# Kernel optimization log

Hardware: AMD Instinct MI355X
Metric: run time of the kernel (lower is better)

## Reference

```python
import jax, jax.numpy as jnp
import numpy as np

HID = 2048; H = 16; QLR = 1536; KVLR = 512
DN = 128; DR = 64; DV = 128; DQ = DN + DR  # 192
B = 2; S = 2048
THETA = 10000.0; EPS = 1e-6


def rms_norm(x, w, eps=EPS):
    x32 = x.astype(jnp.float32)
    var = jnp.mean(x32 * x32, axis=-1, keepdims=True)
    return (w * (x32 * jax.lax.rsqrt(var + eps))).astype(x.dtype)


def rotate_half(x):
    x1, x2 = jnp.split(x, 2, axis=-1)
    return jnp.concatenate((-x2, x1), axis=-1)


def rope_tables(seq_len, dim, base=THETA):
    inv_freq = 1.0 / (base ** (jnp.arange(0, dim, 2, dtype=jnp.float32) / dim))
    t = jnp.arange(seq_len, dtype=jnp.float32)
    freqs = jnp.outer(t, inv_freq)            # [S, dim/2]
    emb = jnp.concatenate((freqs, freqs), -1)  # [S, dim]
    return jnp.cos(emb), jnp.sin(emb)


def setup_inputs() -> dict:
    key = jax.random.key(0)
    ks = jax.random.split(key, 8)
    sd = lambda fan_in: 1.0 / np.sqrt(fan_in)
    return {
        "hidden_states": jax.random.normal(ks[0], (B, S, HID), jnp.float32),
        "w_qa": jax.random.normal(ks[1], (QLR, HID), jnp.float32) * sd(HID),
        "q_a_ln_w": jnp.ones((QLR,), jnp.float32),
        "w_qb": jax.random.normal(ks[2], (H * DQ, QLR), jnp.float32) * sd(QLR),
        "w_kva": jax.random.normal(ks[3], (KVLR + DR, HID), jnp.float32) * sd(HID),
        "kv_a_ln_w": jnp.ones((KVLR,), jnp.float32),
        "w_kvb": jax.random.normal(ks[4], (H * (DN + DV), KVLR), jnp.float32) * sd(KVLR),
        "w_o": jax.random.normal(ks[5], (HID, H * DV), jnp.float32) * sd(H * DV),
    }


def reference(hidden_states, w_qa, q_a_ln_w, w_qb, w_kva, kv_a_ln_w, w_kvb, w_o):
    b, s, _ = hidden_states.shape
    scale = DQ ** -0.5
    cos, sin = rope_tables(s, DR)  # [S, DR] each

    # Q path: low-rank down-proj -> RMSNorm -> up-proj
    cq = rms_norm(hidden_states @ w_qa.T, q_a_ln_w)            # [B,S,QLR]
    q = (cq @ w_qb.T).reshape(b, s, H, DQ).transpose(0, 2, 1, 3)  # [B,H,S,DQ]
    q_nope, q_pe = q[..., :DN], q[..., DN:]
    q_pe = q_pe * cos + rotate_half(q_pe) * sin

    # KV path: joint compressed kv + shared rope key
    ckv = hidden_states @ w_kva.T                               # [B,S,KVLR+DR]
    k_pe = ckv[..., KVLR:].reshape(b, s, 1, DR).transpose(0, 2, 1, 3)  # [B,1,S,DR]
    k_pe = k_pe * cos + rotate_half(k_pe) * sin
    ckv_l = rms_norm(ckv[..., :KVLR], kv_a_ln_w)                # [B,S,KVLR]
    kv = (ckv_l @ w_kvb.T).reshape(b, s, H, DN + DV).transpose(0, 2, 1, 3)
    k_nope, v = kv[..., :DN], kv[..., DN:]                      # [B,H,S,DN],[B,H,S,DV]

    q_full = jnp.concatenate([q_nope, q_pe], axis=-1)           # [B,H,S,DQ]
    k_full = jnp.concatenate(
        [k_nope, jnp.broadcast_to(k_pe, (b, H, s, DR))], axis=-1)

    scores = jnp.einsum('bhqd,bhkd->bhqk', q_full, k_full) * scale
    causal = jnp.triu(jnp.ones((s, s), dtype=bool), k=1)
    scores = jnp.where(causal, -jnp.inf, scores)
    attn = jax.nn.softmax(scores.astype(jnp.float32), axis=-1).astype(q_full.dtype)

    out = jnp.einsum('bhqk,bhkd->bhqd', attn, v)                # [B,H,S,DV]
    out = out.transpose(0, 2, 1, 3).reshape(b, s, H * DV)
    return out @ w_o.T
```

## Files before the change

kernel.cpp:

```cpp
#include <hip/hip_runtime.h>
#include <stdint.h>
#include <stddef.h>

typedef unsigned short u16;
typedef short s16x8 __attribute__((ext_vector_type(8)));
typedef unsigned short u16x4 __attribute__((ext_vector_type(4)));
typedef unsigned short u16x8 __attribute__((ext_vector_type(8)));
typedef float f32x4 __attribute__((ext_vector_type(4)));

__device__ __forceinline__ u16 f2b(float f) {
  uint32_t u = __builtin_bit_cast(uint32_t, f);
  uint32_t r = u + 0x7fffu + ((u >> 16) & 1u);
  return (u16)(r >> 16);
}
__device__ __forceinline__ float b2f(u16 h) {
  uint32_t u = ((uint32_t)h) << 16;
  return __builtin_bit_cast(float, u);
}
__device__ __forceinline__ void gl_lds16(const void* g, void* l) {
  __builtin_amdgcn_global_load_lds((const __attribute__((address_space(1))) void*)g,
                                   (__attribute__((address_space(3))) void*)l,
                                   16, 0, 0);
}

__global__ __launch_bounds__(256) void cast_k(const float* __restrict__ in,
                                              u16* __restrict__ out, int n4) {
  int i = blockIdx.x * 256 + threadIdx.x;
  if (i >= n4) return;
  float4 v = ((const float4*)in)[i];
  u16x4 o; o[0]=f2b(v.x); o[1]=f2b(v.y); o[2]=f2b(v.z); o[3]=f2b(v.w);
  ((u16x4*)out)[i] = o;
}

__global__ __launch_bounds__(256) void cast_pad_k(const float* __restrict__ in,
                                                  u16* __restrict__ out,
                                                  int Kd, int nvalid, int n4) {
  int i = blockIdx.x * 256 + threadIdx.x;
  if (i >= n4) return;
  int row = (i << 2) / Kd;
  u16x4 o;
  if (row < nvalid) {
    float4 v = ((const float4*)in)[i];
    o[0]=f2b(v.x); o[1]=f2b(v.y); o[2]=f2b(v.z); o[3]=f2b(v.w);
  } else {
    o[0]=0; o[1]=0; o[2]=0; o[3]=0;
  }
  ((u16x4*)out)[i] = o;
}

template<int MODE>
__global__ __launch_bounds__(256) void gemm_bt(const u16* __restrict__ A,
                                               const u16* __restrict__ B,
                                               void* __restrict__ Cv,
                                               int M, int N, int K) {
  __shared__ u16 As[128 * 32];
  __shared__ u16 Bs[128 * 32];
  const int t = threadIdx.x;
  const int w = t >> 6, l = t & 63;
  const int nb = N >> 7;
  const int cpx = gridDim.x >> 3;
  const int swz = (blockIdx.x & 7) * cpx + (blockIdx.x >> 3);
  const int bm = (swz / nb) << 7;
  const int bn = (swz % nb) << 7;
  const int wr = (w >> 1) << 6;
  const int wc = (w & 1) << 6;
  const int Kh = K / gridDim.y;
  const int ks0 = blockIdx.y * Kh;

  f32x4 acc[4][4];
  #pragma unroll
  for (int i = 0; i < 4; i++)
    #pragma unroll
    for (int j = 0; j < 4; j++) acc[i][j] = (f32x4){0.f, 0.f, 0.f, 0.f};

  const u16* ga = A + (size_t)(bm + w * 32 + (l >> 2)) * K + ks0 + ((l & 3) * 8);
  const u16* gb = B + (size_t)(bn + w * 32 + (l >> 2)) * K + ks0 + ((l & 3) * 8);
  u16* la0 = &As[(w * 32) * 32];
  u16* la1 = &As[(w * 32 + 16) * 32];
  u16* lb0 = &Bs[(w * 32) * 32];
  u16* lb1 = &Bs[(w * 32 + 16) * 32];

  for (int k0 = 0; k0 < Kh; k0 += 32) {
    __syncthreads();
    gl_lds16(ga, la0);
    gl_lds16(ga + (size_t)16 * K, la1);
    gl_lds16(gb, lb0);
    gl_lds16(gb + (size_t)16 * K, lb1);
    ga += 32; gb += 32;
    __syncthreads();

    s16x8 af[4], bf[4];
    #pragma unroll
    for (int i = 0; i < 4; i++) {
      af[i] = *(const s16x8*)&As[(wr + i * 16 + (l & 15)) * 32 + (l >> 4) * 8];
      bf[i] = *(const s16x8*)&Bs[(wc + i * 16 + (l & 15)) * 32 + (l >> 4) * 8];
    }
    #pragma unroll
    for (int mi = 0; mi < 4; mi++)
      #pragma unroll
      for (int ni = 0; ni < 4; ni++)
        acc[mi][ni] = __builtin_amdgcn_mfma_f32_16x16x32_bf16(af[mi], bf[ni], acc[mi][ni], 0, 0, 0);
  }

  #pragma unroll
  for (int mi = 0; mi < 4; mi++)
    #pragma unroll
    for (int ni = 0; ni < 4; ni++) {
      int row0 = bm + wr + mi * 16 + ((l >> 4) << 2);
      int col  = bn + wc + ni * 16 + (l & 15);
      #pragma unroll
      for (int r = 0; r < 4; r++) {
        float v = acc[mi][ni][r];
        size_t idx = (size_t)(row0 + r) * N + col;
        if (MODE == 1)      ((u16*)Cv)[idx] = f2b(v);
        else if (MODE == 0) ((float*)Cv)[idx] = v;
        else                atomicAdd((float*)Cv + idx, v);
      }
    }
}

__global__ __launch_bounds__(256) void rmsnorm_k(const float* __restrict__ X,
                                                 const float* __restrict__ W,
                                                 u16* __restrict__ Y, int ldx, int D) {
  const int row = blockIdx.x;
  const float* x = X + (size_t)row * ldx;
  const int t = threadIdx.x;
  float ss = 0.f;
  for (int i = t; i < (D >> 2); i += 256) {
    float4 v = ((const float4*)x)[i];
    ss += v.x * v.x + v.y * v.y + v.z * v.z + v.w * v.w;
  }
  #pragma unroll
  for (int off = 32; off > 0; off >>= 1) ss += __shfl_xor(ss, off);
  __shared__ float red[4];
  if ((t & 63) == 0) red[t >> 6] = ss;
  __syncthreads();
  float tot = red[0] + red[1] + red[2] + red[3];
  float r = rsqrtf(tot / (float)D + 1e-6f);
  u16* y = Y + (size_t)row * D;
  for (int i = t; i < (D >> 2); i += 256) {
    float4 v = ((const float4*)x)[i];
    float4 g = ((const float4*)W)[i];
    u16x4 o;
    o[0] = f2b(v.x * r * g.x); o[1] = f2b(v.y * r * g.y);
    o[2] = f2b(v.z * r * g.z); o[3] = f2b(v.w * r * g.w);
    ((u16x4*)y)[i] = o;
  }
}

__global__ __launch_bounds__(256) void rope_kpe_k(const float* __restrict__ CQ,
                                                  u16* __restrict__ Kpe) {
  int idx = blockIdx.x * 256 + threadIdx.x;
  if (idx >= 4096 * 32) return;
  int d = idx & 31;
  int m = idx >> 5;
  int s = m & 2047;
  float inv = expf(-(float)(2 * d) * (9.210340371976184f / 64.0f));
  float ang = (float)s * inv;
  float sn, c;
  sincosf(ang, &sn, &c);
  float x1 = CQ[(size_t)m * 2176 + 2048 + d];
  float x2 = CQ[(size_t)m * 2176 + 2080 + d];
  Kpe[m * 64 + d]      = f2b(x1 * c - x2 * sn);
  Kpe[m * 64 + 32 + d] = f2b(x2 * c + x1 * sn);
}

__global__ __launch_bounds__(256) void rope_q_k(u16* __restrict__ Qb) {
  int idx = blockIdx.x * 256 + threadIdx.x;
  if (idx >= 4096 * 16 * 32) return;
  int d = idx & 31;
  int h = (idx >> 5) & 15;
  int m = idx >> 9;
  int s = m & 2047;
  float inv = expf(-(float)(2 * d) * (9.210340371976184f / 64.0f));
  float ang = (float)s * inv;
  float sn, c;
  sincosf(ang, &sn, &c);
  size_t base = (size_t)m * 3072 + h * 192 + 128 + d;
  float x1 = b2f(Qb[base]);
  float x2 = b2f(Qb[base + 32]);
  Qb[base]      = f2b(x1 * c - x2 * sn);
  Qb[base + 32] = f2b(x2 * c + x1 * sn);
}

__global__ __launch_bounds__(256) void vt_k(const u16* __restrict__ KV,
                                            u16* __restrict__ VT) {
  __shared__ u16 L[64][72];
  const int t = threadIdx.x;
  const int s_t = blockIdx.x & 31;
  const int d_t = (blockIdx.x >> 5) & 1;
  const int bh  = blockIdx.x >> 6;
  const int h = bh & 15, b = bh >> 4;
  const size_t bS = (size_t)b * 2048;
  const int s0 = s_t << 6, d0 = d_t << 6;

  #pragma unroll
  for (int i = 0; i < 2; i++) {
    int rs = (t >> 3) + i * 32;
    int ch = t & 7;
    u16x8 v = *(const u16x8*)&KV[(bS + s0 + rs) * 4096 + h * 256 + 128 + d0 + ch * 8];
    *(u16x8*)&L[rs][ch * 8] = v;
  }
  __syncthreads();
  #pragma unroll
  for (int i = 0; i < 2; i++) {
    int rd = (t >> 3) + i * 32;
    int ch = t & 7;
    u16x8 o;
    #pragma unroll
    for (int j = 0; j < 8; j++) o[j] = L[ch * 8 + j][rd];
    *(u16x8*)&VT[((size_t)bh * 128 + d0 + rd) * 2048 + s0 + ch * 8] = o;
  }
}

__global__ __launch_bounds__(256) void attn4_k(const u16* __restrict__ Q,
                                               const u16* __restrict__ KV,
                                               const u16* __restrict__ Kpe,
                                               const u16* __restrict__ VT,
                                               u16* __restrict__ O) {
  const float SCALE = 0.07216878364870322f;
  const int t = threadIdx.x, w = t >> 6, l = t & 63;
  const int bh = blockIdx.x & 31;
  const int qt = 31 - (blockIdx.x >> 5);
  const int h = bh & 15, b = bh >> 4;
  const int q0 = qt << 6;
  const size_t bS = (size_t)b * 2048;

  __shared__ u16 Kl[2][64 * 192];
  __shared__ u16 Pl[4][16][72];

  s16x8 qf[6];
  {
    const u16* qp = Q + (bS + q0 + w * 16 + (l & 15)) * 3072 + h * 192 + ((l >> 4) * 8);
    #pragma unroll
    for (int c = 0; c < 6; c++) qf[c] = *(const s16x8*)(qp + c * 32);
  }
  float m_i[4] = {-1e30f, -1e30f, -1e30f, -1e30f};
  float lp[4]  = {0.f, 0.f, 0.f, 0.f};
  f32x4 accO[8];
  #pragma unroll
  for (int i = 0; i < 8; i++) accO[i] = (f32x4){0.f, 0.f, 0.f, 0.f};

  const u16* vbp = VT + (size_t)bh * 128 * 2048;
  const int ktiles = qt + 1;

  auto STAGE = [&](int buf, int k0) {
    #pragma unroll
    for (int it = 0; it < 6; ++it) {
      int sl = it * 64 + l;
      int r = w * 16 + sl / 24;
      int cc = (sl % 24) ^ (r & 7);
      const u16* src = (cc < 16)
          ? KV + (bS + k0 + r) * 4096 + h * 256 + cc * 8
          : Kpe + (bS + k0 + r) * 64 + (cc - 16) * 8;
      gl_lds16(src, &Kl[buf][w * 3072 + it * 512]);
    }
  };

  STAGE(0, 0);
  __syncthreads();

  int cur = 0;
  for (int kt = 0; kt < ktiles; ++kt) {
    const int k0 = kt << 6;

    s16x8 va[8], vb[8];
    #pragma unroll
    for (int df = 0; df < 8; df++)
      va[df] = *(const s16x8*)&vbp[(size_t)(df * 16 + (l & 15)) * 2048 + k0 + (l >> 4) * 8];
    #pragma unroll
    for (int df = 0; df < 8; df++)
      vb[df] = *(const s16x8*)&vbp[(size_t)(df * 16 + (l & 15)) * 2048 + k0 + 32 + (l >> 4) * 8];

    if (kt + 1 < ktiles) STAGE(cur ^ 1, k0 + 64);

    f32x4 sa[4];
    #pragma unroll
    for (int cf = 0; cf < 4; cf++) sa[cf] = (f32x4){0.f, 0.f, 0.f, 0.f};
    __builtin_amdgcn_s_setprio(1);
    #pragma unroll
    for (int c = 0; c < 6; c++) {
      #pragma unroll
      for (int cf = 0; cf < 4; cf++) {
        int row = cf * 16 + (l & 15);
        int ch = (c * 4 + (l >> 4)) ^ (row & 7);
        s16x8 kf = *(const s16x8*)&Kl[cur][row * 192 + ch * 8];
        sa[cf] = __builtin_amdgcn_mfma_f32_16x16x32_bf16(qf[c], kf, sa[cf], 0, 0, 0);
      }
    }
    __builtin_amdgcn_s_setprio(0);

    const bool diag = (kt == qt);
    #pragma unroll
    for (int cf = 0; cf < 4; cf++)
      #pragma unroll
      for (int r = 0; r < 4; r++) {
        float s = sa[cf][r] * SCALE;
        if (diag) {
          int qrow = q0 + w * 16 + ((l >> 4) << 2) + r;
          if (k0 + cf * 16 + (l & 15) > qrow) s = -1e30f;
        }
        sa[cf][r] = s;
      }

    float lm[4];
    #pragma unroll
    for (int r = 0; r < 4; r++)
      lm[r] = fmaxf(fmaxf(sa[0][r], sa[1][r]), fmaxf(sa[2][r], sa[3][r]));
    bool safe = (lm[0] <= m_i[0] + 8.f) && (lm[1] <= m_i[1] + 8.f) &&
                (lm[2] <= m_i[2] + 8.f) && (lm[3] <= m_i[3] + 8.f);
    if (!__all(safe)) {
      #pragma unroll
      for (int r = 0; r < 4; r++) {
        float mx = lm[r];
        #pragma unroll
        for (int dd = 1; dd < 16; dd <<= 1) mx = fmaxf(mx, __shfl_xor(mx, dd));
        float mnew = fmaxf(m_i[r], mx);
        float alpha = __expf(m_i[r] - mnew);
        m_i[r] = mnew;
        lp[r] *= alpha;
        #pragma unroll
        for (int df = 0; df < 8; df++) accO[df][r] *= alpha;
      }
    }
    #pragma unroll
    for (int r = 0; r < 4; r++) {
      float e0 = __expf(sa[0][r] - m_i[r]);
      float e1 = __expf(sa[1][r] - m_i[r]);
      float e2 = __expf(sa[2][r] - m_i[r]);
      float e3 = __expf(sa[3][r] - m_i[r]);
      lp[r] += (e0 + e1) + (e2 + e3);
      int prow = ((l >> 4) << 2) + r;
      Pl[w][prow][(l & 15)]      = f2b(e0);
      Pl[w][prow][16 + (l & 15)] = f2b(e1);
      Pl[w][prow][32 + (l & 15)] = f2b(e2);
      Pl[w][prow][48 + (l & 15)] = f2b(e3);
    }

    {
      s16x8 pf0 = *(const s16x8*)&Pl[w][l & 15][(l >> 4) * 8];
      s16x8 pf1 = *(const s16x8*)&Pl[w][l & 15][32 + (l >> 4) * 8];
      __builtin_amdgcn_s_setprio(1);
      #pragma unroll
      for (int df = 0; df < 8; df++)
        accO[df] = __builtin_amdgcn_mfma_f32_16x16x32_bf16(pf0, va[df], accO[df], 0, 0, 0);
      #pragma unroll
      for (int df = 0; df < 8; df++)
        accO[df] = __builtin_amdgcn_mfma_f32_16x16x32_bf16(pf1, vb[df], accO[df], 0, 0, 0);
      __builtin_amdgcn_s_setprio(0);
    }

    __syncthreads();
    cur ^= 1;
  }

  #pragma unroll
  for (int r = 0; r < 4; r++) {
    float s = lp[r];
    #pragma unroll
    for (int dd = 1; dd < 16; dd <<= 1) s += __shfl_xor(s, dd);
    float rl = 1.0f / s;
    #pragma unroll
    for (int df = 0; df < 8; df++) {
      float o = accO[df][r] * rl;
      O[(bS + q0 + w * 16 + ((l >> 4) << 2) + r) * 2048 + h * 128 + df * 16 + (l & 15)] = f2b(o);
    }
  }
}

extern "C" void kernel_launch(void* const* d_in, const int* in_sizes, int n_in,
                              void* d_out, int out_size, void* d_ws, size_t ws_size,
                              hipStream_t stream) {
  const float* hs    = (const float*)d_in[0];
  const float* w_qa  = (const float*)d_in[1];
  const float* q_ln  = (const float*)d_in[2];
  const float* w_qb  = (const float*)d_in[3];
  const float* w_kva = (const float*)d_in[4];
  const float* kv_ln = (const float*)d_in[5];
  const float* w_kvb = (const float*)d_in[6];
  const float* w_o   = (const float*)d_in[7];
  float* out = (float*)d_out;

  char* ws = (char*)d_ws;
  size_t off = 0;
  auto alloc = [&](size_t bytes) -> void* {
    void* p = ws + off;
    off = (off + bytes + 255) & ~(size_t)255;
    return p;
  };
  u16* Xb     = (u16*)alloc(4096ull * 2048 * 2);
  u16* Wcat   = (u16*)alloc(2176ull * 2048 * 2);
  u16* Wqb    = (u16*)alloc(3072ull * 1536 * 2);
  u16* Wkvb   = (u16*)alloc(4096ull * 512 * 2);
  u16* Wo     = (u16*)alloc(2048ull * 2048 * 2);
  float* CQcat = (float*)alloc(4096ull * 2176 * 4);
  u16* CQn    = (u16*)alloc(4096ull * 1536 * 2);
  u16* CKVn   = (u16*)alloc(4096ull * 512 * 2);
  u16* Kpe    = (u16*)alloc(4096ull * 64 * 2);
  u16* KVb    = (u16*)alloc(4096ull * 4096 * 2);
  u16* Ob     = (u16*)alloc(4096ull * 2048 * 2);
  u16* Qb     = (u16*)CQcat;
  u16* VT     = Xb;

  cast_k<<<dim3(8192), 256, 0, stream>>>(hs, Xb, 8388608 / 4);
  cast_k<<<dim3(3072), 256, 0, stream>>>(w_qa, Wcat, 3145728 / 4);
  cast_pad_k<<<dim3(1280), 256, 0, stream>>>(w_kva, Wcat + 1536ull * 2048, 2048, 576, 1310720 / 4);
  cast_k<<<dim3(4608), 256, 0, stream>>>(w_qb, Wqb, 4718592 / 4);
  cast_k<<<dim3(2048), 256, 0, stream>>>(w_kvb, Wkvb, 2097152 / 4);
  cast_k<<<dim3(4096), 256, 0, stream>>>(w_o, Wo, 4194304 / 4);

  hipMemsetAsync(CQcat, 0, 4096ull * 2176 * 4, stream);
  gemm_bt<2><<<dim3(32 * 17, 2), 256, 0, stream>>>(Xb, Wcat, CQcat, 4096, 2176, 2048);

  rmsnorm_k<<<dim3(4096), 256, 0, stream>>>(CQcat, q_ln, CQn, 2176, 1536);
  rmsnorm_k<<<dim3(4096), 256, 0, stream>>>(CQcat + 1536, kv_ln, CKVn, 2176, 512);
  rope_kpe_k<<<dim3(512), 256, 0, stream>>>(CQcat, Kpe);

  gemm_bt<1><<<dim3(32 * 24), 256, 0, stream>>>(CQn, Wqb, Qb, 4096, 3072, 1536);
  gemm_bt<1><<<dim3(32 * 32), 256, 0, stream>>>(CKVn, Wkvb, KVb, 4096, 4096, 512);
  rope_q_k<<<dim3(8192), 256, 0, stream>>>(Qb);

  vt_k<<<dim3(32 * 2 * 32), 256, 0, stream>>>(KVb, VT);

  attn4_k<<<dim3(32 * 32), 256, 0, stream>>>(Qb, KVb, Kpe, VT, Ob);

  hipMemsetAsync(out, 0, 4096ull * 2048 * 4, stream);
  gemm_bt<2><<<dim3(32 * 16, 2), 256, 0, stream>>>(Ob, Wo, out, 4096, 2048, 2048);
}
```

Measured before the change: 623.7 us.

## Shrink attention key tile to 32, split K staging, drop split-K GEMMs

The attention kernel now walks keys in 32-row tiles instead of 64, staged into separate nope and rope LDS buffers. It uses less LDS and fewer registers (launch bounds now request 4 blocks), and causal masking is applied per wave. The final tile is processed partly masked. Separately, the two split-K atomicAdd GEMMs and their memsets are replaced with plain single-pass GEMMs that write directly, removing atomic traffic and zero fills. This halves the grid for those GEMMs, and the smaller attention tiles mean more loop iterations and synchronisations per block.

```diff
diff --git a/kernel.cpp b/kernel.cpp
--- a/kernel.cpp
+++ b/kernel.cpp
@@ -64,8 +64,6 @@
   const int bn = (swz % nb) << 7;
   const int wr = (w >> 1) << 6;
   const int wc = (w & 1) << 6;
-  const int Kh = K / gridDim.y;
-  const int ks0 = blockIdx.y * Kh;
 
   f32x4 acc[4][4];
   #pragma unroll
@@ -73,14 +71,14 @@
     #pragma unroll
     for (int j = 0; j < 4; j++) acc[i][j] = (f32x4){0.f, 0.f, 0.f, 0.f};
 
-  const u16* ga = A + (size_t)(bm + w * 32 + (l >> 2)) * K + ks0 + ((l & 3) * 8);
-  const u16* gb = B + (size_t)(bn + w * 32 + (l >> 2)) * K + ks0 + ((l & 3) * 8);
+  const u16* ga = A + (size_t)(bm + w * 32 + (l >> 2)) * K + ((l & 3) * 8);
+  const u16* gb = B + (size_t)(bn + w * 32 + (l >> 2)) * K + ((l & 3) * 8);
   u16* la0 = &As[(w * 32) * 32];
   u16* la1 = &As[(w * 32 + 16) * 32];
   u16* lb0 = &Bs[(w * 32) * 32];
   u16* lb1 = &Bs[(w * 32 + 16) * 32];
 
-  for (int k0 = 0; k0 < Kh; k0 += 32) {
+  for (int k0 = 0; k0 < K; k0 += 32) {
     __syncthreads();
     gl_lds16(ga, la0);
     gl_lds16(ga + (size_t)16 * K, la1);
@@ -112,9 +110,8 @@
       for (int r = 0; r < 4; r++) {
         float v = acc[mi][ni][r];
         size_t idx = (size_t)(row0 + r) * N + col;
-        if (MODE == 1)      ((u16*)Cv)[idx] = f2b(v);
-        else if (MODE == 0) ((float*)Cv)[idx] = v;
-        else                atomicAdd((float*)Cv + idx, v);
+        if (MODE == 1) ((u16*)Cv)[idx] = f2b(v);
+        else           ((float*)Cv)[idx] = v;
       }
     }
 }
@@ -213,11 +210,11 @@
   }
 }
 
-__global__ __launch_bounds__(256) void attn4_k(const u16* __restrict__ Q,
-                                               const u16* __restrict__ KV,
-                                               const u16* __restrict__ Kpe,
-                                               const u16* __restrict__ VT,
-                                               u16* __restrict__ O) {
+__global__ __launch_bounds__(256, 4) void attn5_k(const u16* __restrict__ Q,
+                                                  const u16* __restrict__ KV,
+                                                  const u16* __restrict__ Kpe,
+                                                  const u16* __restrict__ VT,
+                                                  u16* __restrict__ O) {
   const float SCALE = 0.07216878364870322f;
   const int t = threadIdx.x, w = t >> 6, l = t & 63;
   const int bh = blockIdx.x & 31;
@@ -226,8 +223,9 @@
   const int q0 = qt << 6;
   const size_t bS = (size_t)b * 2048;
 
-  __shared__ u16 Kl[2][64 * 192];
-  __shared__ u16 Pl[4][16][72];
+  __shared__ u16 Kn[2][32 * 128];
+  __shared__ u16 Kp[2][32 * 64];
+  __shared__ u16 Pl[4][16][40];
 
   s16x8 qf[6];
   {
@@ -242,18 +240,20 @@
   for (int i = 0; i < 8; i++) accO[i] = (f32x4){0.f, 0.f, 0.f, 0.f};
 
   const u16* vbp = VT + (size_t)bh * 128 * 2048;
-  const int ktiles = qt + 1;
+  const int ktiles = (q0 >> 5) + 2;
 
   auto STAGE = [&](int buf, int k0) {
     #pragma unroll
-    for (int it = 0; it < 6; ++it) {
-      int sl = it * 64 + l;
-      int r = w * 16 + sl / 24;
-      int cc = (sl % 24) ^ (r & 7);
-      const u16* src = (cc < 16)
-          ? KV + (bS + k0 + r) * 4096 + h * 256 + cc * 8
-          : Kpe + (bS + k0 + r) * 64 + (cc - 16) * 8;
-      gl_lds16(src, &Kl[buf][w * 3072 + it * 512]);
+    for (int it = 0; it < 2; ++it) {
+      int r = it * 16 + w * 4 + (l >> 4);
+      int g = (l & 15) ^ (r & 7);
+      gl_lds16(KV + (bS + k0 + r) * 4096 + h * 256 + g * 8,
+               &Kn[buf][(it * 256 + w * 64) * 8]);
+    }
+    {
+      int r = w * 8 + (l >> 3);
+      int g = (l & 7) ^ (r & 7);
+      gl_lds16(Kpe + (bS + k0 + r) * 64 + g * 8, &Kp[buf][(w * 64) * 8]);
     }
   };
 
@@ -262,51 +262,56 @@
 
   int cur = 0;
   for (int kt = 0; kt < ktiles; ++kt) {
-    const int k0 = kt << 6;
-
-    s16x8 va[8], vb[8];
+    const int k0 = kt << 5;
+
+    s16x8 va[8];
     #pragma unroll
     for (int df = 0; df < 8; df++)
       va[df] = *(const s16x8*)&vbp[(size_t)(df * 16 + (l & 15)) * 2048 + k0 + (l >> 4) * 8];
-    #pragma unroll
-    for (int df = 0; df < 8; df++)
-      vb[df] = *(const s16x8*)&vbp[(size_t)(df * 16 + (l & 15)) * 2048 + k0 + 32 + (l >> 4) * 8];
-
-    if (kt + 1 < ktiles) STAGE(cur ^ 1, k0 + 64);
-
-    f32x4 sa[4];
-    #pragma unroll
-    for (int cf = 0; cf < 4; cf++) sa[cf] = (f32x4){0.f, 0.f, 0.f, 0.f};
-    __builtin_amdgcn_s_setprio(1);
-    #pragma unroll
-    for (int c = 0; c < 6; c++) {
-      #pragma unroll
-      for (int cf = 0; cf < 4; cf++) {
+
+    if (kt + 1 < ktiles) STAGE(cur ^ 1, k0 + 32);
+
+    f32x4 sa[2];
+    sa[0] = (f32x4){0.f, 0.f, 0.f, 0.f};
+    sa[1] = (f32x4){0.f, 0.f, 0.f, 0.f};
+    #pragma unroll
+    for (int c = 0; c < 4; c++) {
+      #pragma unroll
+      for (int cf = 0; cf < 2; cf++) {
         int row = cf * 16 + (l & 15);
         int ch = (c * 4 + (l >> 4)) ^ (row & 7);
-        s16x8 kf = *(const s16x8*)&Kl[cur][row * 192 + ch * 8];
+        s16x8 kf = *(const s16x8*)&Kn[cur][row * 128 + ch * 8];
         sa[cf] = __builtin_amdgcn_mfma_f32_16x16x32_bf16(qf[c], kf, sa[cf], 0, 0, 0);
       }
     }
-    __builtin_amdgcn_s_setprio(0);
-
-    const bool diag = (kt == qt);
-    #pragma unroll
-    for (int cf = 0; cf < 4; cf++)
-      #pragma unroll
-      for (int r = 0; r < 4; r++) {
-        float s = sa[cf][r] * SCALE;
-        if (diag) {
+    #pragma unroll
+    for (int c = 4; c < 6; c++) {
+      #pragma unroll
+      for (int cf = 0; cf < 2; cf++) {
+        int row = cf * 16 + (l & 15);
+        int ch = ((c - 4) * 4 + (l >> 4)) ^ (row & 7);
+        s16x8 kf = *(const s16x8*)&Kp[cur][row * 64 + ch * 8];
+        sa[cf] = __builtin_amdgcn_mfma_f32_16x16x32_bf16(qf[c], kf, sa[cf], 0, 0, 0);
+      }
+    }
+
+    #pragma unroll
+    for (int cf = 0; cf < 2; cf++)
+      #pragma unroll
+      for (int r = 0; r < 4; r++) sa[cf][r] *= SCALE;
+    if (k0 + 32 > q0 + w * 16) {
+      #pragma unroll
+      for (int cf = 0; cf < 2; cf++)
+        #pragma unroll
+        for (int r = 0; r < 4; r++) {
           int qrow = q0 + w * 16 + ((l >> 4) << 2) + r;
-          if (k0 + cf * 16 + (l & 15) > qrow) s = -1e30f;
+          if (k0 + cf * 16 + (l & 15) > qrow) sa[cf][r] = -1e30f;
         }
-        sa[cf][r] = s;
-      }
+    }
 
     float lm[4];
     #pragma unroll
-    for (int r = 0; r < 4; r++)
-      lm[r] = fmaxf(fmaxf(sa[0][r], sa[1][r]), fmaxf(sa[2][r], sa[3][r]));
+    for (int r = 0; r < 4; r++) lm[r] = fmaxf(sa[0][r], sa[1][r]);
     bool safe = (lm[0] <= m_i[0] + 8.f) && (lm[1] <= m_i[1] + 8.f) &&
                 (lm[2] <= m_i[2] + 8.f) && (lm[3] <= m_i[3] + 8.f);
     if (!__all(safe)) {
@@ -327,27 +332,17 @@
     for (int r = 0; r < 4; r++) {
       float e0 = __expf(sa[0][r] - m_i[r]);
       float e1 = __expf(sa[1][r] - m_i[r]);
-      float e2 = __expf(sa[2][r] - m_i[r]);
-      float e3 = __expf(sa[3][r] - m_i[r]);
-      lp[r] += (e0 + e1) + (e2 + e3);
+      lp[r] += e0 + e1;
       int prow = ((l >> 4) << 2) + r;
       Pl[w][prow][(l & 15)]      = f2b(e0);
       Pl[w][prow][16 + (l & 15)] = f2b(e1);
-      Pl[w][prow][32 + (l & 15)] = f2b(e2);
-      Pl[w][prow][48 + (l & 15)] = f2b(e3);
     }
 
     {
-      s16x8 pf0 = *(const s16x8*)&Pl[w][l & 15][(l >> 4) * 8];
-      s16x8 pf1 = *(const s16x8*)&Pl[w][l & 15][32 + (l >> 4) * 8];
-      __builtin_amdgcn_s_setprio(1);
+      s16x8 pf = *(const s16x8*)&Pl[w][l & 15][(l >> 4) * 8];
       #pragma unroll
       for (int df = 0; df < 8; df++)
-        accO[df] = __builtin_amdgcn_mfma_f32_16x16x32_bf16(pf0, va[df], accO[df], 0, 0, 0);
-      #pragma unroll
-      for (int df = 0; df < 8; df++)
-        accO[df] = __builtin_amdgcn_mfma_f32_16x16x32_bf16(pf1, vb[df], accO[df], 0, 0, 0);
-      __builtin_amdgcn_s_setprio(0);
+        accO[df] = __builtin_amdgcn_mfma_f32_16x16x32_bf16(pf, va[df], accO[df], 0, 0, 0);
     }
 
     __syncthreads();
@@ -409,8 +404,7 @@
   cast_k<<<dim3(2048), 256, 0, stream>>>(w_kvb, Wkvb, 2097152 / 4);
   cast_k<<<dim3(4096), 256, 0, stream>>>(w_o, Wo, 4194304 / 4);
 
-  hipMemsetAsync(CQcat, 0, 4096ull * 2176 * 4, stream);
-  gemm_bt<2><<<dim3(32 * 17, 2), 256, 0, stream>>>(Xb, Wcat, CQcat, 4096, 2176, 2048);
+  gemm_bt<0><<<dim3(32 * 17), 256, 0, stream>>>(Xb, Wcat, CQcat, 4096, 2176, 2048);
 
   rmsnorm_k<<<dim3(4096), 256, 0, stream>>>(CQcat, q_ln, CQn, 2176, 1536);
   rmsnorm_k<<<dim3(4096), 256, 0, stream>>>(CQcat + 1536, kv_ln, CKVn, 2176, 512);
@@ -422,8 +416,7 @@
 
   vt_k<<<dim3(32 * 2 * 32), 256, 0, stream>>>(KVb, VT);
 
-  attn4_k<<<dim3(32 * 32), 256, 0, stream>>>(Qb, KVb, Kpe, VT, Ob);
-
-  hipMemsetAsync(out, 0, 4096ull * 2048 * 4, stream);
-  gemm_bt<2><<<dim3(32 * 16, 2), 256, 0, stream>>>(Ob, Wo, out, 4096, 2048, 2048);
-}
+  attn5_k<<<dim3(32 * 32), 256, 0, stream>>>(Qb, KVb, Kpe, VT, Ob);
+
+  gemm_bt<0><<<dim3(32 * 16), 256, 0, stream>>>(Ob, Wo, out, 4096, 2048, 2048);
+}
```

New measurement: 619.2 us. Within noise of the previous version (-0.7%).
